# Performance work log

Hardware: AMD Instinct MI355X
Metric: run time of the kernel (lower is better)

The kernel has to match this reference:

```python
import jax, jax.numpy as jnp
import numpy as np
from math import sqrt

EPS_LN = 1e-5

def _layernorm(x, g, b):
    m = x.mean(-1, keepdims=True)
    v = x.var(-1, keepdims=True)
    return (x - m) / jnp.sqrt(v + EPS_LN) * g + b

def _prob_attn(q, k, v, samp, u):
    # Informer ProbSparse self-attention (single head). q,k,v: [B,L,D], samp: [L,U] sampled key ids.
    B, L, D = q.shape
    k_s = k[:, samp]                                   # [B,L,U,D] sampled keys per query
    qk = jnp.einsum('bld,blud->blu', q, k_s)           # [B,L,U]
    M = qk.max(-1) - qk.mean(-1)                       # sparsity measure [B,L]
    _, top = jax.lax.top_k(M, u)                       # [B,u] active queries
    q_r = jnp.take_along_axis(q, top[..., None], axis=1)         # [B,u,D]
    attn = jax.nn.softmax(jnp.einsum('bud,bld->bul', q_r, k) / sqrt(D), axis=-1)
    upd = jnp.einsum('bul,bld->bud', attn, v)                    # [B,u,D]
    ctx = jnp.broadcast_to(v.mean(axis=1, keepdims=True), (B, L, D))  # lazy queries get mean(V)
    return ctx.at[jnp.arange(B)[:, None], top].set(upd)

def _block(x, p, samp, u):
    # ProbSparse attention block: attn + add&norm + FFN + add&norm
    qw, qb, kw, kb, vw, vb, ow, ob, g1, b1, f1w, f1b, f2w, f2b, g2, b2 = p
    q = x @ qw + qb; k = x @ kw + kb; v = x @ vw + vb
    a = _prob_attn(q, k, v, samp, u) @ ow + ob
    x = _layernorm(x + a, g1, b1)
    ff = jnp.maximum(x @ f1w + f1b, 0.0) @ f2w + f2b
    return _layernorm(x + ff, g2, b2)

def _softpool(x, w1, b1, w2, b2):
    # learned soft-pooling: MLP score per position, softmax over window of 2, weighted sum
    B, L, D = x.shape
    s = jnp.maximum(x @ w1 + b1, 0.0) @ w2 + b2        # [B,L]
    w = jax.nn.softmax(s.reshape(B, L // 2, 2), axis=-1)
    return jnp.einsum('blk,blkd->bld', w, x.reshape(B, L // 2, 2, D))

def _forward(x, pe_w, pe_b, qw, qb, kw, kb, vw, vb, ow, ob, ln1g, ln1b,
             f1w, f1b, f2w, f2b, ln2g, ln2b,
             sp1w1, sp1b1, sp1w2, sp1b2, sp2w1, sp2b1, sp2w2, sp2b2,
             dr_w, dr_b, fc1w, fc1b, fc2w, fc2b, fow, fob,
             samp1, samp2, samp3):
    B, N = x.shape
    normed = x / (x.max() - x.min() + 1e-6)
    h = jnp.stack([x, normed], axis=-1)                # [B,N,2]
    h = h.reshape(B, N // 2, 2, 2).mean(axis=2)        # AvgPool1d(2,2) over length -> [B,148,2]
    L = N // 2
    pos = jnp.arange(L, dtype=h.dtype)
    pe = jnp.stack([jnp.sin(pos), jnp.cos(pos)], axis=-1)  # positionalencoding1d(2, L)
    h = jnp.concatenate([h, jnp.broadcast_to(pe, (B, L, 2))], axis=-1)  # [B,148,4]
    h = h @ pe_w + pe_b                                # [B,148,8]
    us = (25, 25, 20)                                  # factor=5, u = 5*ceil(ln(L))
    samps = (samp1, samp2, samp3)
    for i in range(3):
        p = (qw[i], qb[i], kw[i], kb[i], vw[i], vb[i], ow[i], ob[i],
             ln1g[i], ln1b[i], f1w[i], f1b[i], f2w[i], f2b[i], ln2g[i], ln2b[i])
        h = _block(h, p, samps[i], us[i])
        if i == 0:
            h = _softpool(h, sp1w1, sp1b1, sp1w2, sp1b2)   # 148 -> 74
        if i == 1:
            h = _softpool(h, sp2w1, sp2b1, sp2w2, sp2b2)   # 74 -> 37
    h = h @ dr_w + dr_b                                # Conv1d(8,4,1) == pointwise linear -> [B,37,4]
    h = h.reshape(B, -1)                               # [B,148]
    h = jnp.maximum(h @ fc1w + fc1b, 0.0)
    h = jnp.maximum(h @ fc2w + fc2b, 0.0)
    return jax.nn.sigmoid(h @ fow + fob)               # [B,1]


def setup_inputs() -> dict:
    key = jax.random.key(0)
    ks = iter(jax.random.split(key, 64))
    def n(shape, s=0.1):
        return jax.random.normal(next(ks), shape, jnp.float32) * s
    B, N = 4096, 296
    inp = {}
    inp['x'] = jax.random.normal(next(ks), (B, N), jnp.float32)
    inp['samp1'] = jax.random.randint(next(ks), (148, 25), 0, 148)
    inp['samp2'] = jax.random.randint(next(ks), (74, 25), 0, 74)
    inp['samp3'] = jax.random.randint(next(ks), (37, 20), 0, 37)
    inp['pe_w'], inp['pe_b'] = n((4, 8)), n((8,))
    for name, shape in [('qw', (3, 8, 8)), ('qb', (3, 8)), ('kw', (3, 8, 8)), ('kb', (3, 8)),
                        ('vw', (3, 8, 8)), ('vb', (3, 8)), ('ow', (3, 8, 8)), ('ob', (3, 8)),
                        ('f1w', (3, 8, 12)), ('f1b', (3, 12)), ('f2w', (3, 12, 8)), ('f2b', (3, 8))]:
        inp[name] = n(shape)
    inp['ln1g'] = jnp.ones((3, 8), jnp.float32); inp['ln1b'] = jnp.zeros((3, 8), jnp.float32)
    inp['ln2g'] = jnp.ones((3, 8), jnp.float32); inp['ln2b'] = jnp.zeros((3, 8), jnp.float32)
    for pfx in ('sp1', 'sp2'):
        inp[pfx + 'w1'] = n((8, 12)); inp[pfx + 'b1'] = n((12,))
        inp[pfx + 'w2'] = n((12,));   inp[pfx + 'b2'] = n(())
    inp['dr_w'], inp['dr_b'] = n((8, 4)), n((4,))
    inp['fc1w'], inp['fc1b'] = n((148, 74)), n((74,))
    inp['fc2w'], inp['fc2b'] = n((74, 37)), n((37,))
    inp['fow'], inp['fob'] = n((37, 1)), n((1,))
    return inp


def reference(x, samp1, samp2, samp3, pe_w, pe_b, qw, qb, kw, kb, vw, vb, ow, ob,
              ln1g, ln1b, f1w, f1b, f2w, f2b, ln2g, ln2b,
              sp1w1, sp1b1, sp1w2, sp1b2, sp2w1, sp2b1, sp2w2, sp2b2,
              dr_w, dr_b, fc1w, fc1b, fc2w, fc2b, fow, fob):
    return _forward(x, pe_w, pe_b, qw, qb, kw, kb, vw, vb, ow, ob, ln1g, ln1b,
                    f1w, f1b, f2w, f2b, ln2g, ln2b,
                    sp1w1, sp1b1, sp1w2, sp1b2, sp2w1, sp2b1, sp2w2, sp2b2,
                    dr_w, dr_b, fc1w, fc1b, fc2w, fc2b, fow, fob,
                    samp1, samp2, samp3)
```

## Files before the change

### kernel.cpp

```cpp
#include <hip/hip_runtime.h>
#include <math.h>

#define NTHR 256

struct Params {
    const float* x;
    const int*   samp1;
    const int*   samp2;
    const int*   samp3;
    const float* pe_w; const float* pe_b;
    const float* qw; const float* qb;
    const float* kw; const float* kb;
    const float* vw; const float* vb;
    const float* ow; const float* ob;
    const float* f1w; const float* f1b;
    const float* f2w; const float* f2b;
    const float* ln1g; const float* ln1b;
    const float* ln2g; const float* ln2b;
    const float* sp1w1; const float* sp1b1; const float* sp1w2; const float* sp1b2;
    const float* sp2w1; const float* sp2b1; const float* sp2w2; const float* sp2b2;
    const float* dr_w; const float* dr_b;
    const float* fc1w; const float* fc1b;
    const float* fc2w; const float* fc2b;
    const float* fow;  const float* fob;
    const float* part;
    float* out;
};

__global__ __launch_bounds__(256) void minmax_part(const float4* __restrict__ x4, int n4,
                                                   float* __restrict__ part) {
    float mx = -INFINITY, mn = INFINITY;
    for (int i = blockIdx.x * blockDim.x + threadIdx.x; i < n4; i += gridDim.x * blockDim.x) {
        float4 v = x4[i];
        mx = fmaxf(fmaxf(fmaxf(mx, v.x), fmaxf(v.y, v.z)), v.w);
        mn = fminf(fminf(fminf(mn, v.x), fminf(v.y, v.z)), v.w);
    }
#pragma unroll
    for (int o = 32; o; o >>= 1) {
        mx = fmaxf(mx, __shfl_xor(mx, o));
        mn = fminf(mn, __shfl_xor(mn, o));
    }
    __shared__ float smx[4], smn[4];
    if ((threadIdx.x & 63) == 0) { smx[threadIdx.x >> 6] = mx; smn[threadIdx.x >> 6] = mn; }
    __syncthreads();
    if (threadIdx.x == 0) {
        for (int w = 1; w < 4; ++w) { mx = fmaxf(mx, smx[w]); mn = fminf(mn, smn[w]); }
        part[blockIdx.x * 2]     = mx;
        part[blockIdx.x * 2 + 1] = mn;
    }
}

template<int L, int USAMP, int U, bool POOL>
__device__ __forceinline__ void layer_fn(
    const int t,
    float* __restrict__ h, float* __restrict__ ks, float* __restrict__ vs,
    float* __restrict__ region, float* __restrict__ q_sel, float* __restrict__ upd,
    float* __restrict__ smax, float* __restrict__ ssum, float* __restrict__ vmean,
    int* __restrict__ ntop,
    const float* qw, const float* qb, const float* kw, const float* kb,
    const float* vw, const float* vb, const float* ow, const float* ob,
    const float* f1w, const float* f1b, const float* f2w, const float* f2b,
    const float* g1, const float* bb1, const float* g2, const float* bb2,
    const int* __restrict__ samp,
    const float* spw1, const float* spb1, const float* spw2, const float* spb2)
{
    float* sc = region;
    unsigned long long* keys = (unsigned long long*)region;

    if (t == 0) *ntop = 0;

    float hr[8], qr[8];
    if (t < L) {
#pragma unroll
        for (int e = 0; e < 8; ++e) hr[e] = h[t * 9 + e];
#pragma unroll
        for (int dd = 0; dd < 8; ++dd) {
            float aq = 0.f, ak = 0.f, av = 0.f;
#pragma unroll
            for (int e = 0; e < 8; ++e) {
                aq += hr[e] * qw[e * 8 + dd];
                ak += hr[e] * kw[e * 8 + dd];
                av += hr[e] * vw[e * 8 + dd];
            }
            qr[dd] = aq + qb[dd];
            ks[t * 9 + dd] = ak + kb[dd];
            vs[t * 9 + dd] = av + vb[dd];
        }
    }
    __syncthreads();

    if (t < L) {
        const int* srow = samp + t * USAMP;
        float mx = -INFINITY, sum = 0.f;
        for (int j = 0; j < USAMP; ++j) {
            int idx = srow[j];
            float acc = 0.f;
#pragma unroll
            for (int e = 0; e < 8; ++e) acc += qr[e] * ks[idx * 9 + e];
            mx = fmaxf(mx, acc);
            sum += acc;
        }
        float M = mx - sum / (float)USAMP;
        unsigned ub = __float_as_uint(M);
        ub = (ub & 0x80000000u) ? ~ub : (ub | 0x80000000u);
        keys[t] = ((unsigned long long)ub << 32)
                | (unsigned long long)(0xFFFFFFFFu - (unsigned)t);
    }
    __syncthreads();

    int sj = -1;
    if (t < L) {
        const unsigned long long mykey = keys[t];
        int rank = 0;
#pragma unroll 16
        for (int j = 0; j < L; ++j) rank += (keys[j] > mykey) ? 1 : 0;
        if (rank < U) {
            sj = atomicAdd(ntop, 1);
#pragma unroll
            for (int e = 0; e < 8; ++e) q_sel[sj * 9 + e] = qr[e];
        }
    }
    __syncthreads();

#pragma unroll
    for (int c0 = 0; c0 < U; c0 += 13) {
        const int cn = (U - c0) < 13 ? (U - c0) : 13;

        if (t < L) {
            float kr[8];
#pragma unroll
            for (int e = 0; e < 8; ++e) kr[e] = ks[t * 9 + e];
#pragma unroll
            for (int j = 0; j < cn; ++j) {
                float acc = 0.f;
#pragma unroll
                for (int e = 0; e < 8; ++e) acc += q_sel[(c0 + j) * 9 + e] * kr[e];
                sc[j * 149 + t] = acc * 0.35355339059327373f;
            }
        }
        if (c0 == 0 && t >= 248) {
            int dd = t - 248;
            float acc = 0.f;
#pragma unroll 4
            for (int l = 0; l < L; ++l) acc += vs[l * 9 + dd];
            vmean[dd] = acc / (float)L;
        }
        __syncthreads();

        {
            int g = t >> 3, lg = t & 7;
            if (g < cn) {
                float mx = -INFINITY;
                for (int l = lg; l < L; l += 8) mx = fmaxf(mx, sc[g * 149 + l]);
#pragma unroll
                for (int o = 4; o; o >>= 1) mx = fmaxf(mx, __shfl_xor(mx, o));
                float sm = 0.f;
                for (int l = lg; l < L; l += 8) sm += __expf(sc[g * 149 + l] - mx);
#pragma unroll
                for (int o = 4; o; o >>= 1) sm += __shfl_xor(sm, o);
                if (lg == 0) { smax[g] = mx; ssum[g] = sm; }
            }
        }
        __syncthreads();

        if (t < L) {
#pragma unroll
            for (int j = 0; j < cn; ++j)
                sc[j * 149 + t] = __expf(sc[j * 149 + t] - smax[j]) / ssum[j];
        }
        __syncthreads();

        if (t < cn * 8) {
            int j = t >> 3, dd = t & 7;
            float a0 = 0.f, a1 = 0.f;
#pragma unroll 8
            for (int l = 0; l < (L & ~1); l += 2) {
                a0 += sc[j * 149 + l]     * vs[l * 9 + dd];
                a1 += sc[j * 149 + l + 1] * vs[(l + 1) * 9 + dd];
            }
            float a = a0 + a1;
            if (L & 1) a += sc[j * 149 + (L - 1)] * vs[(L - 1) * 9 + dd];
            upd[(c0 + j) * 9 + dd] = a;
        }
        __syncthreads();
    }

    if (t < L) {
        float ctx[8];
        if (sj >= 0) {
#pragma unroll
            for (int e = 0; e < 8; ++e) ctx[e] = upd[sj * 9 + e];
        } else {
#pragma unroll
            for (int e = 0; e < 8; ++e) ctx[e] = vmean[e];
        }
        float xr[8];
#pragma unroll
        for (int dd = 0; dd < 8; ++dd) {
            float acc = 0.f;
#pragma unroll
            for (int e = 0; e < 8; ++e) acc += ctx[e] * ow[e * 8 + dd];
            xr[dd] = hr[dd] + (acc + ob[dd]);
        }
        float mean = 0.f;
#pragma unroll
        for (int e = 0; e < 8; ++e) mean += xr[e];
        mean *= 0.125f;
        float var = 0.f;
#pragma unroll
        for (int e = 0; e < 8; ++e) { float z = xr[e] - mean; var += z * z; }
        var *= 0.125f;
        float inv = 1.0f / sqrtf(var + 1e-5f);
        float y[8];
#pragma unroll
        for (int e = 0; e < 8; ++e) y[e] = (xr[e] - mean) * inv * g1[e] + bb1[e];

        float f1[12];
#pragma unroll
        for (int o = 0; o < 12; ++o) {
            float acc = 0.f;
#pragma unroll
            for (int e = 0; e < 8; ++e) acc += y[e] * f1w[e * 12 + o];
            f1[o] = fmaxf(acc + f1b[o], 0.f);
        }
        float x2[8];
#pragma unroll
        for (int o = 0; o < 8; ++o) {
            float acc = 0.f;
#pragma unroll
            for (int e = 0; e < 12; ++e) acc += f1[e] * f2w[e * 8 + o];
            x2[o] = y[o] + (acc + f2b[o]);
        }
        mean = 0.f;
#pragma unroll
        for (int e = 0; e < 8; ++e) mean += x2[e];
        mean *= 0.125f;
        var = 0.f;
#pragma unroll
        for (int e = 0; e < 8; ++e) { float z = x2[e] - mean; var += z * z; }
        var *= 0.125f;
        inv = 1.0f / sqrtf(var + 1e-5f);
        float y2[8];
#pragma unroll
        for (int e = 0; e < 8; ++e) {
            y2[e] = (x2[e] - mean) * inv * g2[e] + bb2[e];
            h[t * 9 + e] = y2[e];
        }

        if (POOL) {
            float acc2 = 0.f;
#pragma unroll
            for (int o = 0; o < 12; ++o) {
                float acc = 0.f;
#pragma unroll
                for (int e = 0; e < 8; ++e) acc += y2[e] * spw1[e * 12 + o];
                acc2 += fmaxf(acc + spb1[o], 0.f) * spw2[o];
            }
            region[t] = acc2 + spb2[0];
        }
    }
    __syncthreads();

    if (POOL) {
        constexpr int Lh = L / 2;
        float nrow[8];
        float w0 = 0.f, w1v = 0.f;
        if (t < Lh) {
            float s0 = region[2 * t], s1 = region[2 * t + 1];
            float m = fmaxf(s0, s1);
            float e0 = __expf(s0 - m), e1 = __expf(s1 - m);
            float den = e0 + e1;
            w0 = e0 / den; w1v = e1 / den;
#pragma unroll
            for (int e = 0; e < 8; ++e)
                nrow[e] = w0 * h[(2 * t) * 9 + e] + w1v * h[(2 * t + 1) * 9 + e];
        }
        __syncthreads();
        if (t < Lh) {
#pragma unroll
            for (int e = 0; e < 8; ++e) h[t * 9 + e] = nrow[e];
        }
        __syncthreads();
    }
}

__global__ __launch_bounds__(256, 6) void fused_forward(Params p) {
    const int b = blockIdx.x;
    const int t = threadIdx.x;

    __shared__ float h [148 * 9];
    __shared__ float ks[148 * 9];
    __shared__ float vs[148 * 9];
    __shared__ __align__(16) float region[13 * 149];
    __shared__ float q_sel[25 * 9];
    __shared__ float upd[25 * 9];
    __shared__ float smax[13], ssum[13];
    __shared__ float vmean[8];
    __shared__ int   ntop;
    __shared__ float scale_s;
    __shared__ float smx[4], smn[4];

    {
        float mx = p.part[2 * t], mn = p.part[2 * t + 1];
#pragma unroll
        for (int o = 32; o; o >>= 1) {
            mx = fmaxf(mx, __shfl_xor(mx, o));
            mn = fminf(mn, __shfl_xor(mn, o));
        }
        if ((t & 63) == 0) { smx[t >> 6] = mx; smn[t >> 6] = mn; }
        __syncthreads();
        if (t == 0) {
            for (int w = 1; w < 4; ++w) { mx = fmaxf(mx, smx[w]); mn = fminf(mn, smn[w]); }
            scale_s = mx - mn + 1e-6f;
        }
        __syncthreads();
    }
    const float dscale = scale_s;

    if (t < 148) {
        const float2 xp = ((const float2*)(p.x + b * 296))[t];
        float pin[4];
        pin[0] = 0.5f * (xp.x + xp.y);
        pin[1] = 0.5f * (xp.x / dscale + xp.y / dscale);
        pin[2] = sinf((float)t);
        pin[3] = cosf((float)t);
#pragma unroll
        for (int dd = 0; dd < 8; ++dd) {
            float acc = 0.f;
#pragma unroll
            for (int e = 0; e < 4; ++e) acc += pin[e] * p.pe_w[e * 8 + dd];
            h[t * 9 + dd] = acc + p.pe_b[dd];
        }
    }
    __syncthreads();

    layer_fn<148, 25, 25, true >(t, h, ks, vs, region, q_sel, upd, smax, ssum, vmean, &ntop,
        p.qw,       p.qb,      p.kw,       p.kb,      p.vw,       p.vb,      p.ow,       p.ob,
        p.f1w,      p.f1b,     p.f2w,      p.f2b,
        p.ln1g,     p.ln1b,    p.ln2g,     p.ln2b,    p.samp1,
        p.sp1w1, p.sp1b1, p.sp1w2, p.sp1b2);
    layer_fn<74, 25, 25, true >(t, h, ks, vs, region, q_sel, upd, smax, ssum, vmean, &ntop,
        p.qw + 64,  p.qb + 8,  p.kw + 64,  p.kb + 8,  p.vw + 64,  p.vb + 8,  p.ow + 64,  p.ob + 8,
        p.f1w + 96, p.f1b + 12, p.f2w + 96, p.f2b + 8,
        p.ln1g + 8, p.ln1b + 8, p.ln2g + 8, p.ln2b + 8, p.samp2,
        p.sp2w1, p.sp2b1, p.sp2w2, p.sp2b2);
    layer_fn<37, 20, 20, false>(t, h, ks, vs, region, q_sel, upd, smax, ssum, vmean, &ntop,
        p.qw + 128, p.qb + 16, p.kw + 128, p.kb + 16, p.vw + 128, p.vb + 16, p.ow + 128, p.ob + 16,
        p.f1w + 192, p.f1b + 24, p.f2w + 192, p.f2b + 16,
        p.ln1g + 16, p.ln1b + 16, p.ln2g + 16, p.ln2b + 16, p.samp3,
        nullptr, nullptr, nullptr, nullptr);

    float* hf  = region + 256;
    float* s1b = region;
    float* hd2 = region + 512;
    if (t < 37) {
        float yr[8];
#pragma unroll
        for (int e = 0; e < 8; ++e) yr[e] = h[t * 9 + e];
#pragma unroll
        for (int c = 0; c < 4; ++c) {
            float acc = 0.f;
#pragma unroll
            for (int e = 0; e < 8; ++e) acc += yr[e] * p.dr_w[e * 4 + c];
            hf[t * 4 + c] = acc + p.dr_b[c];
        }
    }
    __syncthreads();
    if (t < 74) {
        float acc = 0.f;
#pragma unroll 4
        for (int i = 0; i < 148; ++i) acc += hf[i] * p.fc1w[i * 74 + t];
        s1b[t] = fmaxf(acc + p.fc1b[t], 0.f);
    }
    __syncthreads();
    if (t < 37) {
        float acc = 0.f;
#pragma unroll 2
        for (int i = 0; i < 74; ++i) acc += s1b[i] * p.fc2w[i * 37 + t];
        hd2[t] = fmaxf(acc + p.fc2b[t], 0.f);
    }
    __syncthreads();
    if (t == 0) {
        float acc = 0.f;
        for (int i = 0; i < 37; ++i) acc += hd2[i] * p.fow[i];
        acc += p.fob[0];
        p.out[b] = 1.f / (1.f + __expf(-acc));
    }
}

extern "C" void kernel_launch(void* const* d_in, const int* in_sizes, int n_in,
                              void* d_out, int out_size, void* d_ws, size_t ws_size,
                              hipStream_t stream) {
    Params p;
    p.x     = (const float*)d_in[0];
    p.samp1 = (const int*)d_in[1];
    p.samp2 = (const int*)d_in[2];
    p.samp3 = (const int*)d_in[3];
    p.pe_w  = (const float*)d_in[4];  p.pe_b  = (const float*)d_in[5];
    p.qw    = (const float*)d_in[6];  p.qb    = (const float*)d_in[7];
    p.kw    = (const float*)d_in[8];  p.kb    = (const float*)d_in[9];
    p.vw    = (const float*)d_in[10]; p.vb    = (const float*)d_in[11];
    p.ow    = (const float*)d_in[12]; p.ob    = (const float*)d_in[13];
    p.f1w   = (const float*)d_in[14]; p.f1b   = (const float*)d_in[15];
    p.f2w   = (const float*)d_in[16]; p.f2b   = (const float*)d_in[17];
    p.ln1g  = (const float*)d_in[18]; p.ln1b  = (const float*)d_in[19];
    p.ln2g  = (const float*)d_in[20]; p.ln2b  = (const float*)d_in[21];
    p.sp1w1 = (const float*)d_in[22]; p.sp1b1 = (const float*)d_in[23];
    p.sp1w2 = (const float*)d_in[24]; p.sp1b2 = (const float*)d_in[25];
    p.sp2w1 = (const float*)d_in[26]; p.sp2b1 = (const float*)d_in[27];
    p.sp2w2 = (const float*)d_in[28]; p.sp2b2 = (const float*)d_in[29];
    p.dr_w  = (const float*)d_in[30]; p.dr_b  = (const float*)d_in[31];
    p.fc1w  = (const float*)d_in[32]; p.fc1b  = (const float*)d_in[33];
    p.fc2w  = (const float*)d_in[34]; p.fc2b  = (const float*)d_in[35];
    p.fow   = (const float*)d_in[36]; p.fob   = (const float*)d_in[37];

    const int n = in_sizes[0];
    const int B = n / 296;

    float* part = (float*)d_ws;

    minmax_part<<<256, 256, 0, stream>>>((const float4*)p.x, n / 4, part);

    p.part = part;
    p.out  = (float*)d_out;
    fused_forward<<<B, 256, 0, stream>>>(p);
}
```

Before: 388.0 us.

## Fuse scores, softmax and PV into per-query lane groups; pad rows for float4

```diff
diff --git a/kernel.cpp b/kernel.cpp
--- a/kernel.cpp
+++ b/kernel.cpp
@@ -1,7 +1,7 @@
 #include <hip/hip_runtime.h>
 #include <math.h>
 
-#define NTHR 256
+#define STR 12
 
 struct Params {
     const float* x;
@@ -50,13 +50,18 @@
     }
 }
 
+__device__ __forceinline__ float dot8(const float4& a, const float4& b,
+                                      const float4& c, const float4& d) {
+    return a.x*c.x + a.y*c.y + a.z*c.z + a.w*c.w
+         + b.x*d.x + b.y*d.y + b.z*d.z + b.w*d.w;
+}
+
 template<int L, int USAMP, int U, bool POOL>
 __device__ __forceinline__ void layer_fn(
     const int t,
     float* __restrict__ h, float* __restrict__ ks, float* __restrict__ vs,
-    float* __restrict__ region, float* __restrict__ q_sel, float* __restrict__ upd,
-    float* __restrict__ smax, float* __restrict__ ssum, float* __restrict__ vmean,
-    int* __restrict__ ntop,
+    unsigned long long* __restrict__ keys, float* __restrict__ q_sel,
+    float* __restrict__ upd, float* __restrict__ vmean, int* __restrict__ ntop,
     const float* qw, const float* qb, const float* kw, const float* kb,
     const float* vw, const float* vb, const float* ow, const float* ob,
     const float* f1w, const float* f1b, const float* f2w, const float* f2b,
@@ -64,143 +69,219 @@
     const int* __restrict__ samp,
     const float* spw1, const float* spb1, const float* spw2, const float* spb2)
 {
-    float* sc = region;
-    unsigned long long* keys = (unsigned long long*)region;
-
     if (t == 0) *ntop = 0;
 
-    float hr[8], qr[8];
+    float hrr[8], qr[8];
     if (t < L) {
-#pragma unroll
-        for (int e = 0; e < 8; ++e) hr[e] = h[t * 9 + e];
+        const float4 ha = *(const float4*)&h[t*STR];
+        const float4 hb = *(const float4*)&h[t*STR+4];
+        hrr[0]=ha.x; hrr[1]=ha.y; hrr[2]=ha.z; hrr[3]=ha.w;
+        hrr[4]=hb.x; hrr[5]=hb.y; hrr[6]=hb.z; hrr[7]=hb.w;
+        float ka[8], va[8];
 #pragma unroll
         for (int dd = 0; dd < 8; ++dd) {
             float aq = 0.f, ak = 0.f, av = 0.f;
 #pragma unroll
             for (int e = 0; e < 8; ++e) {
-                aq += hr[e] * qw[e * 8 + dd];
-                ak += hr[e] * kw[e * 8 + dd];
-                av += hr[e] * vw[e * 8 + dd];
+                aq += hrr[e] * qw[e*8+dd];
+                ak += hrr[e] * kw[e*8+dd];
+                av += hrr[e] * vw[e*8+dd];
             }
             qr[dd] = aq + qb[dd];
-            ks[t * 9 + dd] = ak + kb[dd];
-            vs[t * 9 + dd] = av + vb[dd];
-        }
+            ka[dd] = ak + kb[dd];
+            va[dd] = av + vb[dd];
+        }
+        *(float4*)&ks[t*STR]   = make_float4(ka[0],ka[1],ka[2],ka[3]);
+        *(float4*)&ks[t*STR+4] = make_float4(ka[4],ka[5],ka[6],ka[7]);
+        *(float4*)&vs[t*STR]   = make_float4(va[0],va[1],va[2],va[3]);
+        *(float4*)&vs[t*STR+4] = make_float4(va[4],va[5],va[6],va[7]);
     }
     __syncthreads();
 
     if (t < L) {
         const int* srow = samp + t * USAMP;
         float mx = -INFINITY, sum = 0.f;
+#pragma unroll 5
         for (int j = 0; j < USAMP; ++j) {
-            int idx = srow[j];
-            float acc = 0.f;
-#pragma unroll
-            for (int e = 0; e < 8; ++e) acc += qr[e] * ks[idx * 9 + e];
+            const int idx = srow[j];
+            const float4 ka = *(const float4*)&ks[idx*STR];
+            const float4 kb = *(const float4*)&ks[idx*STR+4];
+            const float acc = qr[0]*ka.x + qr[1]*ka.y + qr[2]*ka.z + qr[3]*ka.w
+                            + qr[4]*kb.x + qr[5]*kb.y + qr[6]*kb.z + qr[7]*kb.w;
             mx = fmaxf(mx, acc);
             sum += acc;
         }
-        float M = mx - sum / (float)USAMP;
+        const float M = mx - sum / (float)USAMP;
         unsigned ub = __float_as_uint(M);
         ub = (ub & 0x80000000u) ? ~ub : (ub | 0x80000000u);
         keys[t] = ((unsigned long long)ub << 32)
                 | (unsigned long long)(0xFFFFFFFFu - (unsigned)t);
+        if ((L & 1) && t == 0) keys[L] = 0ull;
     }
     __syncthreads();
 
     int sj = -1;
     if (t < L) {
         const unsigned long long mykey = keys[t];
+        constexpr int NP = (L + 1) / 2;
+        const ulonglong2* k2 = (const ulonglong2*)keys;
         int rank = 0;
-#pragma unroll 16
-        for (int j = 0; j < L; ++j) rank += (keys[j] > mykey) ? 1 : 0;
+#pragma unroll 8
+        for (int jp = 0; jp < NP; ++jp) {
+            const ulonglong2 kk = k2[jp];
+            rank += (kk.x > mykey) ? 1 : 0;
+            rank += (kk.y > mykey) ? 1 : 0;
+        }
         if (rank < U) {
             sj = atomicAdd(ntop, 1);
-#pragma unroll
-            for (int e = 0; e < 8; ++e) q_sel[sj * 9 + e] = qr[e];
-        }
-    }
-    __syncthreads();
-
-#pragma unroll
-    for (int c0 = 0; c0 < U; c0 += 13) {
-        const int cn = (U - c0) < 13 ? (U - c0) : 13;
-
-        if (t < L) {
-            float kr[8];
-#pragma unroll
-            for (int e = 0; e < 8; ++e) kr[e] = ks[t * 9 + e];
-#pragma unroll
-            for (int j = 0; j < cn; ++j) {
-                float acc = 0.f;
-#pragma unroll
-                for (int e = 0; e < 8; ++e) acc += q_sel[(c0 + j) * 9 + e] * kr[e];
-                sc[j * 149 + t] = acc * 0.35355339059327373f;
-            }
-        }
-        if (c0 == 0 && t >= 248) {
-            int dd = t - 248;
-            float acc = 0.f;
-#pragma unroll 4
-            for (int l = 0; l < L; ++l) acc += vs[l * 9 + dd];
-            vmean[dd] = acc / (float)L;
-        }
-        __syncthreads();
-
-        {
-            int g = t >> 3, lg = t & 7;
-            if (g < cn) {
+            *(float4*)&q_sel[sj*STR]   = make_float4(qr[0],qr[1],qr[2],qr[3]);
+            *(float4*)&q_sel[sj*STR+4] = make_float4(qr[4],qr[5],qr[6],qr[7]);
+        }
+    }
+    __syncthreads();
+
+    {
+        const int w = t >> 6;
+        constexpr int NG = (U > 24) ? 24 : U;
+        if (w < 3) {
+            const int g  = (t >> 3) & 7;
+            const int lg = t & 7;
+            const int j  = w * 8 + g;
+            if (j < NG) {
+                const float4 qa = *(const float4*)&q_sel[j*STR];
+                const float4 qb4 = *(const float4*)&q_sel[j*STR+4];
+                constexpr int NK = (L + 7) / 8;
+                float pk[NK];
                 float mx = -INFINITY;
-                for (int l = lg; l < L; l += 8) mx = fmaxf(mx, sc[g * 149 + l]);
-#pragma unroll
-                for (int o = 4; o; o >>= 1) mx = fmaxf(mx, __shfl_xor(mx, o));
-                float sm = 0.f;
-                for (int l = lg; l < L; l += 8) sm += __expf(sc[g * 149 + l] - mx);
-#pragma unroll
-                for (int o = 4; o; o >>= 1) sm += __shfl_xor(sm, o);
-                if (lg == 0) { smax[g] = mx; ssum[g] = sm; }
-            }
-        }
-        __syncthreads();
-
-        if (t < L) {
-#pragma unroll
-            for (int j = 0; j < cn; ++j)
-                sc[j * 149 + t] = __expf(sc[j * 149 + t] - smax[j]) / ssum[j];
-        }
-        __syncthreads();
-
-        if (t < cn * 8) {
-            int j = t >> 3, dd = t & 7;
-            float a0 = 0.f, a1 = 0.f;
-#pragma unroll 8
-            for (int l = 0; l < (L & ~1); l += 2) {
-                a0 += sc[j * 149 + l]     * vs[l * 9 + dd];
-                a1 += sc[j * 149 + l + 1] * vs[(l + 1) * 9 + dd];
-            }
-            float a = a0 + a1;
-            if (L & 1) a += sc[j * 149 + (L - 1)] * vs[(L - 1) * 9 + dd];
-            upd[(c0 + j) * 9 + dd] = a;
-        }
-        __syncthreads();
-    }
+#pragma unroll
+                for (int k = 0; k < NK; ++k) {
+                    const int l = lg + 8*k;
+                    float s = -INFINITY;
+                    if (l < L) {
+                        const float4 ka = *(const float4*)&ks[l*STR];
+                        const float4 kb = *(const float4*)&ks[l*STR+4];
+                        s = dot8(qa, qb4, ka, kb) * 0.35355339059327373f;
+                    }
+                    pk[k] = s;
+                    mx = fmaxf(mx, s);
+                }
+                mx = fmaxf(mx, __shfl_xor(mx, 1, 8));
+                mx = fmaxf(mx, __shfl_xor(mx, 2, 8));
+                mx = fmaxf(mx, __shfl_xor(mx, 4, 8));
+                float acc[8] = {0,0,0,0,0,0,0,0};
+                float ssum = 0.f;
+#pragma unroll
+                for (int k = 0; k < NK; ++k) {
+                    const int l = lg + 8*k;
+                    if (l < L) {
+                        const float e = __expf(pk[k] - mx);
+                        ssum += e;
+                        const float4 va = *(const float4*)&vs[l*STR];
+                        const float4 vb = *(const float4*)&vs[l*STR+4];
+                        acc[0] += e*va.x; acc[1] += e*va.y; acc[2] += e*va.z; acc[3] += e*va.w;
+                        acc[4] += e*vb.x; acc[5] += e*vb.y; acc[6] += e*vb.z; acc[7] += e*vb.w;
+                    }
+                }
+#pragma unroll
+                for (int m = 1; m <= 4; m <<= 1) {
+                    ssum += __shfl_xor(ssum, m, 8);
+#pragma unroll
+                    for (int d = 0; d < 8; ++d) acc[d] += __shfl_xor(acc[d], m, 8);
+                }
+                if (lg == 0) {
+#pragma unroll
+                    for (int d = 0; d < 8; ++d) upd[j*STR + d] = acc[d] / ssum;
+                }
+            }
+        } else {
+            const int m64 = t & 63;
+            constexpr int NK64 = (L + 63) / 64;
+            float vacc[8] = {0,0,0,0,0,0,0,0};
+            float acc[8]  = {0,0,0,0,0,0,0,0};
+            float ssum = 0.f;
+            float pk[NK64];
+            float mx = -INFINITY;
+            float4 qa = make_float4(0,0,0,0), qb4 = make_float4(0,0,0,0);
+            if constexpr (U > 24) {
+                qa  = *(const float4*)&q_sel[24*STR];
+                qb4 = *(const float4*)&q_sel[24*STR+4];
+            }
+#pragma unroll
+            for (int k = 0; k < NK64; ++k) {
+                const int l = m64 + 64*k;
+                float s = -INFINITY;
+                if constexpr (U > 24) {
+                    if (l < L) {
+                        const float4 ka = *(const float4*)&ks[l*STR];
+                        const float4 kb = *(const float4*)&ks[l*STR+4];
+                        s = dot8(qa, qb4, ka, kb) * 0.35355339059327373f;
+                    }
+                }
+                pk[k] = s;
+                mx = fmaxf(mx, s);
+            }
+            if constexpr (U > 24) {
+#pragma unroll
+                for (int m = 1; m <= 32; m <<= 1) mx = fmaxf(mx, __shfl_xor(mx, m));
+            }
+#pragma unroll
+            for (int k = 0; k < NK64; ++k) {
+                const int l = m64 + 64*k;
+                if (l < L) {
+                    const float4 va = *(const float4*)&vs[l*STR];
+                    const float4 vb = *(const float4*)&vs[l*STR+4];
+                    vacc[0] += va.x; vacc[1] += va.y; vacc[2] += va.z; vacc[3] += va.w;
+                    vacc[4] += vb.x; vacc[5] += vb.y; vacc[6] += vb.z; vacc[7] += vb.w;
+                    if constexpr (U > 24) {
+                        const float e = __expf(pk[k] - mx);
+                        ssum += e;
+                        acc[0] += e*va.x; acc[1] += e*va.y; acc[2] += e*va.z; acc[3] += e*va.w;
+                        acc[4] += e*vb.x; acc[5] += e*vb.y; acc[6] += e*vb.z; acc[7] += e*vb.w;
+                    }
+                }
+            }
+#pragma unroll
+            for (int m = 1; m <= 32; m <<= 1) {
+#pragma unroll
+                for (int d = 0; d < 8; ++d) vacc[d] += __shfl_xor(vacc[d], m);
+                if constexpr (U > 24) {
+                    ssum += __shfl_xor(ssum, m);
+#pragma unroll
+                    for (int d = 0; d < 8; ++d) acc[d] += __shfl_xor(acc[d], m);
+                }
+            }
+            if (m64 == 0) {
+#pragma unroll
+                for (int d = 0; d < 8; ++d) vmean[d] = vacc[d] / (float)L;
+                if constexpr (U > 24) {
+#pragma unroll
+                    for (int d = 0; d < 8; ++d) upd[24*STR + d] = acc[d] / ssum;
+                }
+            }
+        }
+    }
+    __syncthreads();
 
     if (t < L) {
         float ctx[8];
         if (sj >= 0) {
-#pragma unroll
-            for (int e = 0; e < 8; ++e) ctx[e] = upd[sj * 9 + e];
+            const float4 ua = *(const float4*)&upd[sj*STR];
+            const float4 ub4 = *(const float4*)&upd[sj*STR+4];
+            ctx[0]=ua.x; ctx[1]=ua.y; ctx[2]=ua.z; ctx[3]=ua.w;
+            ctx[4]=ub4.x; ctx[5]=ub4.y; ctx[6]=ub4.z; ctx[7]=ub4.w;
         } else {
-#pragma unroll
-            for (int e = 0; e < 8; ++e) ctx[e] = vmean[e];
+            const float4 va = *(const float4*)&vmean[0];
+            const float4 vb = *(const float4*)&vmean[4];
+            ctx[0]=va.x; ctx[1]=va.y; ctx[2]=va.z; ctx[3]=va.w;
+            ctx[4]=vb.x; ctx[5]=vb.y; ctx[6]=vb.z; ctx[7]=vb.w;
         }
         float xr[8];
 #pragma unroll
         for (int dd = 0; dd < 8; ++dd) {
             float acc = 0.f;
 #pragma unroll
-            for (int e = 0; e < 8; ++e) acc += ctx[e] * ow[e * 8 + dd];
-            xr[dd] = hr[dd] + (acc + ob[dd]);
+            for (int e = 0; e < 8; ++e) acc += ctx[e] * ow[e*8+dd];
+            xr[dd] = hrr[dd] + (acc + ob[dd]);
         }
         float mean = 0.f;
 #pragma unroll
@@ -208,7 +289,7 @@
         mean *= 0.125f;
         float var = 0.f;
 #pragma unroll
-        for (int e = 0; e < 8; ++e) { float z = xr[e] - mean; var += z * z; }
+        for (int e = 0; e < 8; ++e) { const float z = xr[e] - mean; var += z*z; }
         var *= 0.125f;
         float inv = 1.0f / sqrtf(var + 1e-5f);
         float y[8];
@@ -220,7 +301,7 @@
         for (int o = 0; o < 12; ++o) {
             float acc = 0.f;
 #pragma unroll
-            for (int e = 0; e < 8; ++e) acc += y[e] * f1w[e * 12 + o];
+            for (int e = 0; e < 8; ++e) acc += y[e] * f1w[e*12+o];
             f1[o] = fmaxf(acc + f1b[o], 0.f);
         }
         float x2[8];
@@ -228,7 +309,7 @@
         for (int o = 0; o < 8; ++o) {
             float acc = 0.f;
 #pragma unroll
-            for (int e = 0; e < 12; ++e) acc += f1[e] * f2w[e * 8 + o];
+            for (int e = 0; e < 12; ++e) acc += f1[e] * f2w[e*8+o];
             x2[o] = y[o] + (acc + f2b[o]);
         }
         mean = 0.f;
@@ -237,15 +318,14 @@
         mean *= 0.125f;
         var = 0.f;
 #pragma unroll
-        for (int e = 0; e < 8; ++e) { float z = x2[e] - mean; var += z * z; }
+        for (int e = 0; e < 8; ++e) { const float z = x2[e] - mean; var += z*z; }
         var *= 0.125f;
         inv = 1.0f / sqrtf(var + 1e-5f);
         float y2[8];
 #pragma unroll
-        for (int e = 0; e < 8; ++e) {
-            y2[e] = (x2[e] - mean) * inv * g2[e] + bb2[e];
-            h[t * 9 + e] = y2[e];
-        }
+        for (int e = 0; e < 8; ++e) y2[e] = (x2[e] - mean) * inv * g2[e] + bb2[e];
+        *(float4*)&h[t*STR]   = make_float4(y2[0],y2[1],y2[2],y2[3]);
+        *(float4*)&h[t*STR+4] = make_float4(y2[4],y2[5],y2[6],y2[7]);
 
         if (POOL) {
             float acc2 = 0.f;
@@ -253,10 +333,10 @@
             for (int o = 0; o < 12; ++o) {
                 float acc = 0.f;
 #pragma unroll
-                for (int e = 0; e < 8; ++e) acc += y2[e] * spw1[e * 12 + o];
+                for (int e = 0; e < 8; ++e) acc += y2[e] * spw1[e*12+o];
                 acc2 += fmaxf(acc + spb1[o], 0.f) * spw2[o];
             }
-            region[t] = acc2 + spb2[0];
+            ((float*)keys)[t] = acc2 + spb2[0];
         }
     }
     __syncthreads();
@@ -264,44 +344,48 @@
     if (POOL) {
         constexpr int Lh = L / 2;
         float nrow[8];
-        float w0 = 0.f, w1v = 0.f;
+        const float* spsc = (const float*)keys;
         if (t < Lh) {
-            float s0 = region[2 * t], s1 = region[2 * t + 1];
-            float m = fmaxf(s0, s1);
-            float e0 = __expf(s0 - m), e1 = __expf(s1 - m);
-            float den = e0 + e1;
-            w0 = e0 / den; w1v = e1 / den;
-#pragma unroll
-            for (int e = 0; e < 8; ++e)
-                nrow[e] = w0 * h[(2 * t) * 9 + e] + w1v * h[(2 * t + 1) * 9 + e];
+            const float2 ss = *(const float2*)&spsc[2*t];
+            const float m = fmaxf(ss.x, ss.y);
+            const float e0 = __expf(ss.x - m), e1 = __expf(ss.y - m);
+            const float den = e0 + e1;
+            const float w0 = e0 / den, w1 = e1 / den;
+            const float4 a0 = *(const float4*)&h[(2*t)*STR];
+            const float4 a1 = *(const float4*)&h[(2*t)*STR+4];
+            const float4 b0 = *(const float4*)&h[(2*t+1)*STR];
+            const float4 b1 = *(const float4*)&h[(2*t+1)*STR+4];
+            nrow[0] = w0*a0.x + w1*b0.x; nrow[1] = w0*a0.y + w1*b0.y;
+            nrow[2] = w0*a0.z + w1*b0.z; nrow[3] = w0*a0.w + w1*b0.w;
+            nrow[4] = w0*a1.x + w1*b1.x; nrow[5] = w0*a1.y + w1*b1.y;
+            nrow[6] = w0*a1.z + w1*b1.z; nrow[7] = w0*a1.w + w1*b1.w;
         }
         __syncthreads();
         if (t < Lh) {
-#pragma unroll
-            for (int e = 0; e < 8; ++e) h[t * 9 + e] = nrow[e];
+            *(float4*)&h[t*STR]   = make_float4(nrow[0],nrow[1],nrow[2],nrow[3]);
+            *(float4*)&h[t*STR+4] = make_float4(nrow[4],nrow[5],nrow[6],nrow[7]);
         }
         __syncthreads();
     }
 }
 
-__global__ __launch_bounds__(256, 6) void fused_forward(Params p) {
+__global__ __launch_bounds__(256, 4) void fused_forward(Params p) {
     const int b = blockIdx.x;
     const int t = threadIdx.x;
 
-    __shared__ float h [148 * 9];
-    __shared__ float ks[148 * 9];
-    __shared__ float vs[148 * 9];
-    __shared__ __align__(16) float region[13 * 149];
-    __shared__ float q_sel[25 * 9];
-    __shared__ float upd[25 * 9];
-    __shared__ float smax[13], ssum[13];
-    __shared__ float vmean[8];
+    __shared__ __align__(16) float h [148 * STR];
+    __shared__ __align__(16) float ks[148 * STR];
+    __shared__ __align__(16) float vs[148 * STR];
+    __shared__ __align__(16) unsigned long long keys[150];
+    __shared__ __align__(16) float q_sel[25 * STR];
+    __shared__ __align__(16) float upd[25 * STR];
+    __shared__ __align__(16) float vmean[8];
     __shared__ int   ntop;
     __shared__ float scale_s;
     __shared__ float smx[4], smn[4];
 
     {
-        float mx = p.part[2 * t], mn = p.part[2 * t + 1];
+        float mx = p.part[2*t], mn = p.part[2*t+1];
 #pragma unroll
         for (int o = 32; o; o >>= 1) {
             mx = fmaxf(mx, __shfl_xor(mx, o));
@@ -324,67 +408,76 @@
         pin[1] = 0.5f * (xp.x / dscale + xp.y / dscale);
         pin[2] = sinf((float)t);
         pin[3] = cosf((float)t);
+        float o[8];
 #pragma unroll
         for (int dd = 0; dd < 8; ++dd) {
             float acc = 0.f;
 #pragma unroll
-            for (int e = 0; e < 4; ++e) acc += pin[e] * p.pe_w[e * 8 + dd];
-            h[t * 9 + dd] = acc + p.pe_b[dd];
-        }
-    }
-    __syncthreads();
-
-    layer_fn<148, 25, 25, true >(t, h, ks, vs, region, q_sel, upd, smax, ssum, vmean, &ntop,
-        p.qw,       p.qb,      p.kw,       p.kb,      p.vw,       p.vb,      p.ow,       p.ob,
-        p.f1w,      p.f1b,     p.f2w,      p.f2b,
-        p.ln1g,     p.ln1b,    p.ln2g,     p.ln2b,    p.samp1,
+            for (int e = 0; e < 4; ++e) acc += pin[e] * p.pe_w[e*8+dd];
+            o[dd] = acc + p.pe_b[dd];
+        }
+        *(float4*)&h[t*STR]   = make_float4(o[0],o[1],o[2],o[3]);
+        *(float4*)&h[t*STR+4] = make_float4(o[4],o[5],o[6],o[7]);
+    }
+    __syncthreads();
+
+    layer_fn<148, 25, 25, true >(t, h, ks, vs, keys, q_sel, upd, vmean, &ntop,
+        p.qw,       p.qb,       p.kw,       p.kb,       p.vw,       p.vb,       p.ow,       p.ob,
+        p.f1w,      p.f1b,      p.f2w,      p.f2b,
+        p.ln1g,     p.ln1b,     p.ln2g,     p.ln2b,     p.samp1,
         p.sp1w1, p.sp1b1, p.sp1w2, p.sp1b2);
-    layer_fn<74, 25, 25, true >(t, h, ks, vs, region, q_sel, upd, smax, ssum, vmean, &ntop,
-        p.qw + 64,  p.qb + 8,  p.kw + 64,  p.kb + 8,  p.vw + 64,  p.vb + 8,  p.ow + 64,  p.ob + 8,
+    layer_fn<74, 25, 25, true >(t, h, ks, vs, keys, q_sel, upd, vmean, &ntop,
+        p.qw + 64,  p.qb + 8,   p.kw + 64,  p.kb + 8,   p.vw + 64,  p.vb + 8,   p.ow + 64,  p.ob + 8,
         p.f1w + 96, p.f1b + 12, p.f2w + 96, p.f2b + 8,
         p.ln1g + 8, p.ln1b + 8, p.ln2g + 8, p.ln2b + 8, p.samp2,
         p.sp2w1, p.sp2b1, p.sp2w2, p.sp2b2);
-    layer_fn<37, 20, 20, false>(t, h, ks, vs, region, q_sel, upd, smax, ssum, vmean, &ntop,
-        p.qw + 128, p.qb + 16, p.kw + 128, p.kb + 16, p.vw + 128, p.vb + 16, p.ow + 128, p.ob + 16,
+    layer_fn<37, 20, 20, false>(t, h, ks, vs, keys, q_sel, upd, vmean, &ntop,
+        p.qw + 128, p.qb + 16,  p.kw + 128, p.kb + 16,  p.vw + 128, p.vb + 16,  p.ow + 128, p.ob + 16,
         p.f1w + 192, p.f1b + 24, p.f2w + 192, p.f2b + 16,
         p.ln1g + 16, p.ln1b + 16, p.ln2g + 16, p.ln2b + 16, p.samp3,
         nullptr, nullptr, nullptr, nullptr);
 
-    float* hf  = region + 256;
-    float* s1b = region;
-    float* hd2 = region + 512;
+    float* hf  = ks;
+    float* s1  = vs;
+    float* hd2 = (float*)q_sel;
     if (t < 37) {
-        float yr[8];
-#pragma unroll
-        for (int e = 0; e < 8; ++e) yr[e] = h[t * 9 + e];
+        const float4 ya = *(const float4*)&h[t*STR];
+        const float4 yb = *(const float4*)&h[t*STR+4];
+        float o[4];
 #pragma unroll
         for (int c = 0; c < 4; ++c) {
-            float acc = 0.f;
-#pragma unroll
-            for (int e = 0; e < 8; ++e) acc += yr[e] * p.dr_w[e * 4 + c];
-            hf[t * 4 + c] = acc + p.dr_b[c];
-        }
+            float acc = ya.x*p.dr_w[0*4+c] + ya.y*p.dr_w[1*4+c]
+                      + ya.z*p.dr_w[2*4+c] + ya.w*p.dr_w[3*4+c]
+                      + yb.x*p.dr_w[4*4+c] + yb.y*p.dr_w[5*4+c]
+                      + yb.z*p.dr_w[6*4+c] + yb.w*p.dr_w[7*4+c];
+            o[c] = acc + p.dr_b[c];
+        }
+        *(float4*)&hf[t*4] = make_float4(o[0],o[1],o[2],o[3]);
     }
     __syncthreads();
     if (t < 74) {
         float acc = 0.f;
 #pragma unroll 4
-        for (int i = 0; i < 148; ++i) acc += hf[i] * p.fc1w[i * 74 + t];
-        s1b[t] = fmaxf(acc + p.fc1b[t], 0.f);
+        for (int i4 = 0; i4 < 37; ++i4) {
+            const float4 hv = *(const float4*)&hf[i4*4];
+            const int i = i4 * 4;
+            acc += hv.x * p.fc1w[(i  )*74 + t] + hv.y * p.fc1w[(i+1)*74 + t]
+                 + hv.z * p.fc1w[(i+2)*74 + t] + hv.w * p.fc1w[(i+3)*74 + t];
+        }
+        s1[t] = fmaxf(acc + p.fc1b[t], 0.f);
     }
     __syncthreads();
     if (t < 37) {
         float acc = 0.f;
 #pragma unroll 2
-        for (int i = 0; i < 74; ++i) acc += s1b[i] * p.fc2w[i * 37 + t];
+        for (int i = 0; i < 74; ++i) acc += s1[i] * p.fc2w[i*37 + t];
         hd2[t] = fmaxf(acc + p.fc2b[t], 0.f);
     }
     __syncthreads();
     if (t == 0) {
         float acc = 0.f;
         for (int i = 0; i < 37; ++i) acc += hd2[i] * p.fow[i];
-        acc += p.fob[0];
-        p.out[b] = 1.f / (1.f + __expf(-acc));
+        p.out[b] = 1.f / (1.f + __expf(-(acc + p.fob[0])));
     }
 }
 
```

Measured after the change: 406.1 us. 1.05x slower.
